# Kernel optimization log

Hardware: AMD Instinct MI355X
Metric: run time of the kernel (lower is better)

The kernel has to match this reference:

```python
import jax, jax.numpy as jnp
import numpy as np

PERIOD = 25
ADJUST = True
ALPHA = 2.0 / (PERIOD + 1.0)


def setup_inputs() -> dict:
    key = jax.random.key(0)
    x = jax.random.normal(key, (32, 4096, 256), dtype=jnp.float32)
    return {"x": x}


def reference(x):
    # x: (B, T, F). Faithful to the keras layer: EMA_0 = x_0;
    # for t>=1: e_t = (alpha*x_t + (1-alpha)*e_{t-1}) / max(1-(1-alpha)^(t+1), 1e-10)
    # (the bias-corrected value is fed back into the recurrence, matching the source).
    B, T, F = x.shape
    alpha = jnp.asarray(ALPHA, x.dtype)
    oma = jnp.asarray(1.0 - ALPHA, x.dtype)

    if ADJUST:
        t = jnp.arange(1, T, dtype=x.dtype)  # t = 1..T-1
        w = jnp.maximum(1.0 - oma ** (t + 1.0), jnp.asarray(1e-10, x.dtype))  # (T-1,)
    else:
        w = jnp.ones((T - 1,), dtype=x.dtype)

    e0 = x[:, 0, :]                      # (B, F)
    xs = jnp.swapaxes(x[:, 1:, :], 0, 1)  # (T-1, B, F), time-major for scan

    def step(e_prev, inp):
        x_t, w_t = inp
        e = (alpha * x_t + oma * e_prev) / w_t
        return e, e

    _, es = jax.lax.scan(step, e0, (xs, w))  # es: (T-1, B, F)
    ema = jnp.concatenate([e0[:, None, :], jnp.swapaxes(es, 0, 1)], axis=1)
    return ema
```

## Files before the change

### kernel.cpp

```cpp
#include <hip/hip_runtime.h>
#include <math.h>


namespace {

constexpr int kT = 4096;
constexpr int kF4 = 64;
constexpr int kL = 64;
constexpr int kHalo = 128;
constexpr int kNC = kT / kL;
constexpr int kG = 16;
constexpr int kBatches = 32;
constexpr int kBlocks = kBatches * kNC;

constexpr double kAlphaD = 2.0 / 26.0;
constexpr float kAlpha = (float)kAlphaD;
constexpr float kOma   = (float)(1.0 - kAlphaD);

__device__ __forceinline__ void load_group(const float4* __restrict__ p,
                                           float4 (&buf)[kG]) {
#pragma unroll
  for (int i = 0; i < kG; ++i) buf[i] = p[i * kF4];
}

__device__ __forceinline__ void store_group(float4* __restrict__ p,
                                            const float4 (&buf)[kG]) {
#pragma unroll
  for (int i = 0; i < kG; ++i) p[i * kF4] = buf[i];
}

__device__ __forceinline__ void step_fast(float4& e, const float4 v) {
  e.x = fmaf(kOma, e.x, kAlpha * v.x);
  e.y = fmaf(kOma, e.y, kAlpha * v.y);
  e.z = fmaf(kOma, e.z, kAlpha * v.z);
  e.w = fmaf(kOma, e.w, kAlpha * v.w);
}

template <bool EXACT>
__device__ __forceinline__ void process_group(float4 (&buf)[kG], float4& e,
                                              double& p, int tbase) {
#pragma unroll
  for (int i = 0; i < kG; ++i) {
    const float4 v = buf[i];
    if (EXACT) {
      if (tbase + i == 0) {
        e = v;
      } else {
        p *= (double)kOma;
        const float w = fmaxf(1.0f - (float)p, 1e-10f);
        const float inv = 1.0f / w;
        step_fast(e, v);
        e.x *= inv; e.y *= inv; e.z *= inv; e.w *= inv;
      }
    } else {
      step_fast(e, v);
    }
    buf[i] = e;
  }
}

template <bool EXACT>
__device__ __forceinline__ void run_chunk(const float4* __restrict__ px,
                                          float4* __restrict__ po,
                                          int ng, int hg, int t0) {
  float4 e = make_float4(0.f, 0.f, 0.f, 0.f);
  float4 bufA[kG], bufB[kG];
  double p = 0.0;
  if (EXACT) {
    p = pow((double)kOma, (double)t0);
    if (t0 == 0) p = 1.0;
  }
  if (EXACT) p = pow((double)kOma, (double)(t0 == 0 ? 1 : t0));

  load_group(px, bufA);
  px += kG * kF4;
  for (int g = 0; g < ng; g += 2) {
    load_group(px, bufB);
    px += kG * kF4;
    process_group<EXACT>(bufA, e, p, t0 + g * kG);
    if (g >= hg) {
      store_group(po, bufA);
      po += kG * kF4;
    }
    if (g + 2 < ng) {
      load_group(px, bufA);
      px += kG * kF4;
    }
    process_group<EXACT>(bufB, e, p, t0 + (g + 1) * kG);
    if (g + 1 >= hg) {
      store_group(po, bufB);
      po += kG * kF4;
    }
  }
}

}

__global__ __launch_bounds__(64, 2) void ema_kernel(const float* __restrict__ x,
                                                    float* __restrict__ out) {
  const int sw = (blockIdx.x & 7) * (kBlocks / 8) + (blockIdx.x >> 3);
  const int b = sw / kNC;
  const int c = sw & (kNC - 1);

  const int t0 = (c >= 2) ? (c * kL - kHalo) : 0;
  const int rows = (c == 0) ? kL : (c == 1 ? 2 * kL : kHalo + kL);
  const int ng = rows / kG;
  const int hg = (c * kL - t0) / kG;

  const float4* px = reinterpret_cast<const float4*>(x) +
                     ((size_t)b * kT + t0) * kF4 + threadIdx.x;
  float4* po = reinterpret_cast<float4*>(out) +
               ((size_t)b * kT + (size_t)c * kL) * kF4 + threadIdx.x;

  if (c < 6) {
    run_chunk<true>(px, po, ng, hg, t0);
  } else {
    run_chunk<false>(px, po, ng, hg, t0);
  }
}

extern "C" void kernel_launch(void* const* d_in, const int* in_sizes, int n_in,
                              void* d_out, int out_size, void* d_ws, size_t ws_size,
                              hipStream_t stream) {
  (void)in_sizes; (void)n_in; (void)d_ws; (void)ws_size; (void)out_size;
  const float* x = reinterpret_cast<const float*>(d_in[0]);
  float* out = reinterpret_cast<float*>(d_out);
  hipLaunchKernelGGL(ema_kernel, dim3(kBlocks), dim3(64), 0, stream, x, out);
}
```

Baseline: 257.2 us.

## Use longer chunks with shorter halo, float2 lanes, and nontemporal stores

Chunks grow from 64 to 256 timesteps and the warm-up halo shrinks from 128 to 64 rows, so far less input is re-read for halo recomputation. Each block now runs 128 threads with float2 per thread instead of 64 threads with float4, and outputs are written with nontemporal stores. The exact bias-corrected path now runs only for the first chunk, which is valid because the correction factor has converged by t=256. The shorter halo relies on (1-alpha)^64 decay being small enough to keep accuracy, and there are fewer blocks, which may lower parallelism.

```diff
diff --git a/kernel.cpp b/kernel.cpp
--- a/kernel.cpp
+++ b/kernel.cpp
@@ -1,15 +1,16 @@
 #include <hip/hip_runtime.h>
-#include <math.h>
 
 
 namespace {
 
+typedef float f2 __attribute__((ext_vector_type(2)));
+
 constexpr int kT = 4096;
-constexpr int kF4 = 64;
-constexpr int kL = 64;
-constexpr int kHalo = 128;
+constexpr int kF2 = 128;
+constexpr int kL = 256;
+constexpr int kHalo = 64;
 constexpr int kNC = kT / kL;
-constexpr int kG = 16;
+constexpr int kG = 32;
 constexpr int kBatches = 32;
 constexpr int kBlocks = kBatches * kNC;
 
@@ -17,31 +18,30 @@
 constexpr float kAlpha = (float)kAlphaD;
 constexpr float kOma   = (float)(1.0 - kAlphaD);
 
-__device__ __forceinline__ void load_group(const float4* __restrict__ p,
-                                           float4 (&buf)[kG]) {
+__device__ __forceinline__ void load_group(const f2* __restrict__ p,
+                                           f2 (&buf)[kG]) {
 #pragma unroll
-  for (int i = 0; i < kG; ++i) buf[i] = p[i * kF4];
+  for (int i = 0; i < kG; ++i) buf[i] = p[(size_t)i * kF2];
 }
 
-__device__ __forceinline__ void store_group(float4* __restrict__ p,
-                                            const float4 (&buf)[kG]) {
+__device__ __forceinline__ void store_group(f2* __restrict__ p,
+                                            const f2 (&buf)[kG]) {
 #pragma unroll
-  for (int i = 0; i < kG; ++i) p[i * kF4] = buf[i];
+  for (int i = 0; i < kG; ++i)
+    __builtin_nontemporal_store(buf[i], p + (size_t)i * kF2);
 }
 
-__device__ __forceinline__ void step_fast(float4& e, const float4 v) {
+__device__ __forceinline__ void step_fast(f2& e, const f2 v) {
   e.x = fmaf(kOma, e.x, kAlpha * v.x);
   e.y = fmaf(kOma, e.y, kAlpha * v.y);
-  e.z = fmaf(kOma, e.z, kAlpha * v.z);
-  e.w = fmaf(kOma, e.w, kAlpha * v.w);
 }
 
 template <bool EXACT>
-__device__ __forceinline__ void process_group(float4 (&buf)[kG], float4& e,
+__device__ __forceinline__ void process_group(f2 (&buf)[kG], f2& e,
                                               double& p, int tbase) {
 #pragma unroll
   for (int i = 0; i < kG; ++i) {
-    const float4 v = buf[i];
+    const f2 v = buf[i];
     if (EXACT) {
       if (tbase + i == 0) {
         e = v;
@@ -50,7 +50,7 @@
         const float w = fmaxf(1.0f - (float)p, 1e-10f);
         const float inv = 1.0f / w;
         step_fast(e, v);
-        e.x *= inv; e.y *= inv; e.z *= inv; e.w *= inv;
+        e.x *= inv; e.y *= inv;
       }
     } else {
       step_fast(e, v);
@@ -60,62 +60,55 @@
 }
 
 template <bool EXACT>
-__device__ __forceinline__ void run_chunk(const float4* __restrict__ px,
-                                          float4* __restrict__ po,
+__device__ __forceinline__ void run_chunk(const f2* __restrict__ px,
+                                          f2* __restrict__ po,
                                           int ng, int hg, int t0) {
-  float4 e = make_float4(0.f, 0.f, 0.f, 0.f);
-  float4 bufA[kG], bufB[kG];
-  double p = 0.0;
-  if (EXACT) {
-    p = pow((double)kOma, (double)t0);
-    if (t0 == 0) p = 1.0;
-  }
-  if (EXACT) p = pow((double)kOma, (double)(t0 == 0 ? 1 : t0));
+  f2 e = {0.f, 0.f};
+  f2 bufA[kG], bufB[kG];
+  double p = (double)kOma;
 
   load_group(px, bufA);
-  px += kG * kF4;
+  px += (size_t)kG * kF2;
   for (int g = 0; g < ng; g += 2) {
     load_group(px, bufB);
-    px += kG * kF4;
+    px += (size_t)kG * kF2;
     process_group<EXACT>(bufA, e, p, t0 + g * kG);
     if (g >= hg) {
       store_group(po, bufA);
-      po += kG * kF4;
+      po += (size_t)kG * kF2;
     }
     if (g + 2 < ng) {
       load_group(px, bufA);
-      px += kG * kF4;
+      px += (size_t)kG * kF2;
     }
     process_group<EXACT>(bufB, e, p, t0 + (g + 1) * kG);
     if (g + 1 >= hg) {
       store_group(po, bufB);
-      po += kG * kF4;
+      po += (size_t)kG * kF2;
     }
   }
 }
 
 }
 
-__global__ __launch_bounds__(64, 2) void ema_kernel(const float* __restrict__ x,
-                                                    float* __restrict__ out) {
+__global__ __launch_bounds__(128) void ema_kernel(const float* __restrict__ x,
+                                                  float* __restrict__ out) {
   const int sw = (blockIdx.x & 7) * (kBlocks / 8) + (blockIdx.x >> 3);
   const int b = sw / kNC;
   const int c = sw & (kNC - 1);
+  const int tid = threadIdx.x;
 
-  const int t0 = (c >= 2) ? (c * kL - kHalo) : 0;
-  const int rows = (c == 0) ? kL : (c == 1 ? 2 * kL : kHalo + kL);
-  const int ng = rows / kG;
-  const int hg = (c * kL - t0) / kG;
-
-  const float4* px = reinterpret_cast<const float4*>(x) +
-                     ((size_t)b * kT + t0) * kF4 + threadIdx.x;
-  float4* po = reinterpret_cast<float4*>(out) +
-               ((size_t)b * kT + (size_t)c * kL) * kF4 + threadIdx.x;
-
-  if (c < 6) {
-    run_chunk<true>(px, po, ng, hg, t0);
+  if (c == 0) {
+    const f2* px = reinterpret_cast<const f2*>(x) + (size_t)b * kT * kF2 + tid;
+    f2* po = reinterpret_cast<f2*>(out) + (size_t)b * kT * kF2 + tid;
+    run_chunk<true>(px, po, kL / kG , 0, 0);
   } else {
-    run_chunk<false>(px, po, ng, hg, t0);
+    const int t0 = c * kL - kHalo;
+    const f2* px = reinterpret_cast<const f2*>(x) +
+                   ((size_t)b * kT + t0) * kF2 + tid;
+    f2* po = reinterpret_cast<f2*>(out) +
+             ((size_t)b * kT + (size_t)c * kL) * kF2 + tid;
+    run_chunk<false>(px, po, (kL + kHalo) / kG , kHalo / kG , t0);
   }
 }
 
@@ -125,5 +118,5 @@
   (void)in_sizes; (void)n_in; (void)d_ws; (void)ws_size; (void)out_size;
   const float* x = reinterpret_cast<const float*>(d_in[0]);
   float* out = reinterpret_cast<float*>(d_out);
-  hipLaunchKernelGGL(ema_kernel, dim3(kBlocks), dim3(64), 0, stream, x, out);
+  hipLaunchKernelGGL(ema_kernel, dim3(kBlocks), dim3(128), 0, stream, x, out);
 }
```

Result: faster. 240.8 us (-6.4%).
